# Performance work log

Hardware: AMD Instinct MI355X
Metric: run time of the kernel (lower is better)

Reference implementation:

```python
import jax, jax.numpy as jnp
import numpy as np
from jax import lax

SZ, SENLEN, V, DWE, DPE, MAXPOS, DEE, DR, DC, KLOC = 2048, 128, 50000, 100, 5, 256, 100, 34, 300, 10
CIN = DWE + 2 * DPE + DEE  # 210


def setup_inputs() -> dict:
    key = jax.random.key(0)
    ks = jax.random.split(key, 16)
    inp = jax.random.randint(ks[0], (SZ, SENLEN), 0, V, dtype=jnp.int32)
    pos1 = jax.random.randint(ks[1], (SZ, SENLEN), 0, MAXPOS, dtype=jnp.int32)
    pos2 = jax.random.randint(ks[2], (SZ, SENLEN), 0, MAXPOS, dtype=jnp.int32)
    loc = jax.random.randint(ks[3], (SZ, KLOC), 0, V, dtype=jnp.int32)
    loc_mark = jax.random.randint(ks[4], (SZ,), 1, 6, dtype=jnp.int32)  # 1..5, keeps 4+mark < KLOC
    subtype = jax.random.randint(ks[5], (SZ,), 0, DR, dtype=jnp.int32)
    # piecewise L/M/R sentence masks around two cut points
    a = jax.random.randint(ks[6], (SZ, 1), 1, SENLEN // 2, dtype=jnp.int32)
    b = jax.random.randint(ks[7], (SZ, 1), SENLEN // 2, SENLEN - 1, dtype=jnp.int32)
    ar = jnp.arange(SENLEN)[None, :]
    maskL = (ar < a).astype(jnp.float32)
    maskM = ((ar >= a) & (ar < b)).astype(jnp.float32)
    maskR = (ar >= b).astype(jnp.float32)
    word_emb = 0.1 * jax.random.normal(ks[8], (V, DWE), dtype=jnp.float32)
    pos_emb = 0.1 * jax.random.normal(ks[9], (MAXPOS, DPE), dtype=jnp.float32)
    event_emb = 0.1 * jax.random.normal(ks[10], (DR, DEE), dtype=jnp.float32)
    conv_w = (1.0 / np.sqrt(CIN * 3)) * jax.random.normal(ks[11], (DC, CIN, 3), dtype=jnp.float32)
    conv_b = 0.01 * jax.random.normal(ks[12], (DC,), dtype=jnp.float32)
    return dict(inp=inp, pos1=pos1, pos2=pos2, loc=loc, loc_mark=loc_mark, subtype=subtype,
                maskL=maskL, maskM=maskM, maskR=maskR, word_emb=word_emb, pos_emb=pos_emb,
                event_emb=event_emb, conv_w=conv_w, conv_b=conv_b)


def reference(inp, pos1, pos2, loc, loc_mark, subtype, maskL, maskM, maskR,
              word_emb, pos_emb, event_emb, conv_w, conv_b):
    # padding_idx=0 semantics
    W = word_emb.at[0].set(0.0)
    E = event_emb.at[0].set(0.0)

    embeds = W[inp]                       # (SZ, L, DWE)
    p1 = pos_emb[pos1]                    # (SZ, L, DPE)
    p2 = pos_emb[pos2]                    # (SZ, L, DPE)

    # ragged loc feature: l[4] <- mean(l[4:4+mark]); l[5] <- l[4+mark]; keep l[0:6]
    loc_e = W[loc]                        # (SZ, K, DWE)
    j = jnp.arange(KLOC)[None, :]
    sel = ((j >= 4) & (j < 4 + loc_mark[:, None])).astype(loc_e.dtype)  # (SZ, K)
    mean4 = jnp.einsum('skd,sk->sd', loc_e, sel) / loc_mark[:, None].astype(loc_e.dtype)
    new5 = jnp.take_along_axis(loc_e, (4 + loc_mark)[:, None, None], axis=1)[:, 0, :]
    loc_embeds = jnp.concatenate([loc_e[:, :4].reshape(loc_e.shape[0], -1), mean4, new5], axis=1)  # (SZ, 6*DWE)

    ev = jnp.broadcast_to(E[subtype][:, None, :], (subtype.shape[0], SENLEN, DEE))
    x = jnp.concatenate([embeds, p1, p2, ev], axis=2).transpose(0, 2, 1)  # (SZ, CIN, L)

    conved = lax.conv_general_dilated(x, conv_w, window_strides=(1,), padding=((1, 1),),
                                      dimension_numbers=('NCH', 'OIH', 'NCH'))
    conved = conved + conv_b[None, :, None]  # (SZ, DC, L)

    # (mask*x + 1) -> maxpool over L -> -1  ==  max over L of mask*x (the +/-1 cancels exactly)
    pooledL = jnp.max(conved * maskL[:, None, :], axis=2)
    pooledM = jnp.max(conved * maskM[:, None, :], axis=2)
    pooledR = jnp.max(conved * maskR[:, None, :], axis=2)
    pooled = jnp.concatenate([pooledL, pooledM, pooledR], axis=1)  # (SZ, 3*DC)

    rep = jnp.tanh(jnp.concatenate([pooled, loc_embeds], axis=1))  # dropout in eval = identity
    return rep
```

## Files before the change

### kernel.cpp

```cpp
#include <hip/hip_runtime.h>
#include <hip/hip_bf16.h>

#define SZ    2048
#define SLEN  128
#define DWE   100
#define DPE   5
#define DEE   100
#define DC    300
#define CIN   210
#define KLOC  10
#define OUTW  1500
#define DR    34

#define KP    128
#define LCOLS 136
#define LROWS 130
#define CPAD  320

typedef short short8 __attribute__((ext_vector_type(8)));
typedef float f32x4 __attribute__((ext_vector_type(4)));

static __device__ __forceinline__ unsigned short f2b(float f) {
  return __builtin_bit_cast(unsigned short, __float2bfloat16(f));
}

static __device__ __forceinline__ unsigned cvt_pk_bf16(float lo, float hi) {
  unsigned r;
  asm volatile("v_cvt_pk_bf16_f32 %0, %1, %2" : "=v"(r) : "v"(lo), "v"(hi));
  return r;
}

static __device__ __forceinline__ float ftanh(float x) {
  x = fminf(fmaxf(x, -15.f), 15.f);
  float e = __expf(2.0f * x);
  return (e - 1.0f) * __builtin_amdgcn_rcpf(e + 1.0f);
}

__global__ void prep_wk(const float* __restrict__ conv_w, unsigned short* __restrict__ wk) {
  int idx = blockIdx.x * 256 + threadIdx.x;
  if (idx >= 3 * CPAD * KP) return;
  int i  = idx & (KP - 1);
  int c  = (idx / KP) % CPAD;
  int kk = idx / (KP * CPAD);
  float v = 0.f;
  if (c < DC && i < 110) v = conv_w[(c * CIN + i) * 3 + kk];
  wk[idx] = f2b(v);
}

__global__ void prep_ev(const float* __restrict__ conv_w, const float* __restrict__ event_emb,
                        const float* __restrict__ conv_b, float* __restrict__ evconv) {
  int gid = blockIdx.x * 256 + threadIdx.x;
  int o = gid >> 2, sub = gid & 3;
  if (o >= DR * 3 * DC) return;
  int c  = o % DC;
  int kk = (o / DC) % 3;
  int st = o / (3 * DC);
  float v = 0.f;
  if (st != 0) {
    const float* wrow = conv_w + (c * CIN + 110) * 3 + kk;
    const float* e = event_emb + st * DEE;
    #pragma unroll
    for (int i = 0; i < 25; ++i) v += wrow[3 * (sub * 25 + i)] * e[sub * 25 + i];
  }
  v += __shfl_xor(v, 1);
  v += __shfl_xor(v, 2);
  if (sub == 0) evconv[o] = v + (kk == 1 ? conv_b[c] : 0.f);
}

__global__ __launch_bounds__(512, 4) void dmcnn_main(
    const int* __restrict__ inp, const int* __restrict__ pos1, const int* __restrict__ pos2,
    const int* __restrict__ loc, const int* __restrict__ loc_mark, const int* __restrict__ subtype,
    const float* __restrict__ maskL, const float* __restrict__ maskM, const float* __restrict__ maskR,
    const float* __restrict__ word_emb, const float* __restrict__ pos_emb,
    const unsigned short* __restrict__ wk, const float* __restrict__ evconv,
    float* __restrict__ out)
{
  __shared__ unsigned short XT[LROWS * LCOLS];
  __shared__ float pool[2 * CPAD * 4];
  __shared__ int cw[4];

  const int s   = blockIdx.x;
  const int tid = threadIdx.x;

  if (tid < 64)        ((unsigned*)XT)[tid] = 0u;
  else if (tid < 128)  ((unsigned*)(XT + 129 * LCOLS))[tid - 64] = 0u;

  if (tid < 128) {
    const int inL = maskL[s * SLEN + tid] > 0.5f;
    const int inM = maskM[s * SLEN + tid] > 0.5f;
    unsigned long long bL = __ballot(inL);
    unsigned long long bM = __ballot(inM);
    if ((tid & 63) == 0) {
      cw[tid >> 6]       = __popcll(bL);
      cw[2 + (tid >> 6)] = __popcll(bM);
    }
  }

  {
    const int t = tid >> 2, q = tid & 3;
    unsigned short* row = &XT[(t + 1) * LCOLS];
    const int w = inp[s * SLEN + t];
    const float4* wp = (const float4*)(word_emb + (size_t)w * DWE);
    for (int j = q; j < 25; j += 4) {
      float4 v = wp[j];
      unsigned lo = cvt_pk_bf16(v.x, v.y);
      unsigned hi = cvt_pk_bf16(v.z, v.w);
      if (w == 0) { lo = 0u; hi = 0u; }
      *(uint2*)&row[4 * j] = make_uint2(lo, hi);
    }
    if (q == 1 || q == 2) {
      const int p = (q == 1 ? pos1 : pos2)[s * SLEN + t];
      const float* pp = pos_emb + p * DPE;
      #pragma unroll
      for (int d = 0; d < DPE; ++d) row[DWE + (q - 1) * DPE + d] = f2b(pp[d]);
    } else if (q == 3) {
      #pragma unroll
      for (int d = 0; d < 9; ++d) *(unsigned*)&row[110 + 2 * d] = 0u;
    }
  }
  __syncthreads();

  const int wv   = tid >> 6;
  const int wc   = wv & 3, wt = wv >> 2;
  const int lane = tid & 63;
  const int r16  = lane & 15, q16 = lane >> 4;

  f32x4 acc[4][5];
  #pragma unroll
  for (int tt = 0; tt < 4; ++tt)
    #pragma unroll
    for (int ci = 0; ci < 5; ++ci) acc[tt][ci] = (f32x4){0.f, 0.f, 0.f, 0.f};

  const unsigned short* wbase = wk + (size_t)(80 * wc + r16) * KP + q16 * 8;
  #pragma unroll 1
  for (int ks = 0; ks < 12; ++ks) {
    const int kk = ks >> 2, kt = ks & 3;
    short8 wf[5];
    #pragma unroll
    for (int ci = 0; ci < 5; ++ci)
      wf[ci] = *(const short8*)(wbase + (size_t)(kk * CPAD + 16 * ci) * KP + kt * 32);
    #pragma unroll
    for (int tt = 0; tt < 4; ++tt) {
      short8 xf = *(const short8*)&XT[(64 * wt + 16 * tt + r16 + kk) * LCOLS + kt * 32 + q16 * 8];
      #pragma unroll
      for (int ci = 0; ci < 5; ++ci)
        acc[tt][ci] = __builtin_amdgcn_mfma_f32_16x16x32_bf16(xf, wf[ci], acc[tt][ci], 0, 0, 0);
    }
  }

  const int acut = cw[0] + cw[1];
  const int bcut = acut + cw[2] + cw[3];
  const int st   = subtype[s];
  const float* evc = evconv + (size_t)st * 3 * DC;
  float* orow = out + (size_t)s * OUTW;

  #pragma unroll
  for (int ci = 0; ci < 5; ++ci) {
    const int c = 80 * wc + 16 * ci + r16;
    const int cc = c < DC ? c : 0;
    const float s0 = evc[cc], s1 = evc[cc + DC], s2 = evc[cc + 2 * DC];
    const float base = s0 + s1 + s2;
    float rL = 0.f, rM = 0.f, rR = 0.f;
    #pragma unroll
    for (int tt = 0; tt < 4; ++tt) {
      #pragma unroll
      for (int j = 0; j < 4; ++j) {
        const int t = 64 * wt + 16 * tt + 4 * q16 + j;
        float v = acc[tt][ci][j] + base;
        if (t == 0)   v -= s0;
        if (t == 127) v -= s2;
        if (t < acut)      rL = fmaxf(rL, v);
        else if (t < bcut) rM = fmaxf(rM, v);
        else               rR = fmaxf(rR, v);
      }
    }
    #pragma unroll
    for (int off = 16; off < 64; off <<= 1) {
      rL = fmaxf(rL, __shfl_xor(rL, off));
      rM = fmaxf(rM, __shfl_xor(rM, off));
      rR = fmaxf(rR, __shfl_xor(rR, off));
    }
    if (q16 == 0) {
      float* p = pool + ((size_t)wt * CPAD + c) * 4;
      p[0] = rL; p[1] = rM; p[2] = rR;
    }
  }

  __syncthreads();
  if (tid < DC) {
    const float* p0 = pool + (size_t)tid * 4;
    const float* p1 = pool + (size_t)(CPAD + tid) * 4;
    orow[tid]          = ftanh(fmaxf(p0[0], p1[0]));
    orow[DC + tid]     = ftanh(fmaxf(p0[1], p1[1]));
    orow[2 * DC + tid] = ftanh(fmaxf(p0[2], p1[2]));
  }

  const int mark = loc_mark[s];
  for (int j = tid; j < 600; j += 512) {
    float v;
    if (j < 400) {
      const int k = j / 100, d = j % 100;
      const int idx = loc[s * KLOC + k];
      v = (idx == 0) ? 0.f : word_emb[(size_t)idx * DWE + d];
    } else if (j < 500) {
      const int d = j - 400;
      float sum = 0.f;
      for (int k = 4; k < 4 + mark; ++k) {
        const int idx = loc[s * KLOC + k];
        sum += (idx == 0) ? 0.f : word_emb[(size_t)idx * DWE + d];
      }
      v = sum / (float)mark;
    } else {
      const int d = j - 500;
      const int idx = loc[s * KLOC + 4 + mark];
      v = (idx == 0) ? 0.f : word_emb[(size_t)idx * DWE + d];
    }
    orow[900 + j] = ftanh(v);
  }
}

extern "C" void kernel_launch(void* const* d_in, const int* in_sizes, int n_in,
                              void* d_out, int out_size, void* d_ws, size_t ws_size,
                              hipStream_t stream) {
  const int*   inp       = (const int*)d_in[0];
  const int*   pos1      = (const int*)d_in[1];
  const int*   pos2      = (const int*)d_in[2];
  const int*   loc       = (const int*)d_in[3];
  const int*   loc_mark  = (const int*)d_in[4];
  const int*   subtype   = (const int*)d_in[5];
  const float* maskL     = (const float*)d_in[6];
  const float* maskM     = (const float*)d_in[7];
  const float* maskR     = (const float*)d_in[8];
  const float* word_emb  = (const float*)d_in[9];
  const float* pos_emb   = (const float*)d_in[10];
  const float* event_emb = (const float*)d_in[11];
  const float* conv_w    = (const float*)d_in[12];
  const float* conv_b    = (const float*)d_in[13];

  unsigned short* wk = (unsigned short*)d_ws;
  float* evconv = (float*)((char*)d_ws + 3 * CPAD * KP * 2);
  float* out = (float*)d_out;

  prep_wk<<<(3 * CPAD * KP + 255) / 256, 256, 0, stream>>>(conv_w, wk);
  prep_ev<<<(DR * 3 * DC * 4 + 255) / 256, 256, 0, stream>>>(conv_w, event_emb, conv_b, evconv);
  dmcnn_main<<<SZ, 512, 0, stream>>>(inp, pos1, pos2, loc, loc_mark, subtype,
      maskL, maskM, maskR, word_emb, pos_emb, wk, evconv, out);
}
```

Baseline: 248.2 us.

## Process multiple sentences per block with software-pipelined gathers and separate loc kernel

The main kernel becomes persistent-style: each block handles eight sentences in sequence, prefetching the next sentence's embedding rows, position embeddings, masks and subtype into registers while the MFMA convolution of the current one runs. The loc-feature tanh work moves to its own elementwise kernel, and launch bounds drop to two blocks per CU. This is meant to hide gather latency and amortise block setup, but the grid shrinks to 256 blocks, which may leave CUs underused, and the prefetch registers add pressure.

Result: slower. 273.6 us (+10.2%).

```diff
diff --git a/kernel.cpp b/kernel.cpp
--- a/kernel.cpp
+++ b/kernel.cpp
@@ -16,6 +16,7 @@
 #define LCOLS 136
 #define LROWS 130
 #define CPAD  320
+#define G     8
 
 typedef short short8 __attribute__((ext_vector_type(8)));
 typedef float f32x4 __attribute__((ext_vector_type(4)));
@@ -67,155 +68,226 @@
   if (sub == 0) evconv[o] = v + (kk == 1 ? conv_b[c] : 0.f);
 }
 
-__global__ __launch_bounds__(512, 4) void dmcnn_main(
+__global__ void loc_kernel(const int* __restrict__ loc, const int* __restrict__ loc_mark,
+                           const float* __restrict__ word_emb, float* __restrict__ out) {
+  int gid = blockIdx.x * 256 + threadIdx.x;
+  if (gid >= SZ * 600) return;
+  int s = gid / 600, j = gid % 600;
+  const int mark = loc_mark[s];
+  float v;
+  if (j < 400) {
+    const int k = j / 100, d = j % 100;
+    const int idx = loc[s * KLOC + k];
+    v = (idx == 0) ? 0.f : word_emb[(size_t)idx * DWE + d];
+  } else if (j < 500) {
+    const int d = j - 400;
+    float sum = 0.f;
+    for (int k = 4; k < 4 + mark; ++k) {
+      const int idx = loc[s * KLOC + k];
+      sum += (idx == 0) ? 0.f : word_emb[(size_t)idx * DWE + d];
+    }
+    v = sum / (float)mark;
+  } else {
+    const int d = j - 500;
+    const int idx = loc[s * KLOC + 4 + mark];
+    v = (idx == 0) ? 0.f : word_emb[(size_t)idx * DWE + d];
+  }
+  out[(size_t)s * OUTW + 900 + j] = ftanh(v);
+}
+
+__global__ __launch_bounds__(512, 2) void dmcnn_main(
     const int* __restrict__ inp, const int* __restrict__ pos1, const int* __restrict__ pos2,
-    const int* __restrict__ loc, const int* __restrict__ loc_mark, const int* __restrict__ subtype,
-    const float* __restrict__ maskL, const float* __restrict__ maskM, const float* __restrict__ maskR,
+    const int* __restrict__ subtype,
+    const float* __restrict__ maskL, const float* __restrict__ maskM,
     const float* __restrict__ word_emb, const float* __restrict__ pos_emb,
     const unsigned short* __restrict__ wk, const float* __restrict__ evconv,
     float* __restrict__ out)
 {
   __shared__ unsigned short XT[LROWS * LCOLS];
-  __shared__ float pool[2 * CPAD * 4];
-  __shared__ int cw[4];
-
-  const int s   = blockIdx.x;
+  __shared__ float pool[2 * 304 * 3];
+  __shared__ int cwbuf[2][4];
+
   const int tid = threadIdx.x;
-
-  if (tid < 64)        ((unsigned*)XT)[tid] = 0u;
-  else if (tid < 128)  ((unsigned*)(XT + 129 * LCOLS))[tid - 64] = 0u;
-
-  if (tid < 128) {
-    const int inL = maskL[s * SLEN + tid] > 0.5f;
-    const int inM = maskM[s * SLEN + tid] > 0.5f;
-    unsigned long long bL = __ballot(inL);
-    unsigned long long bM = __ballot(inM);
-    if ((tid & 63) == 0) {
-      cw[tid >> 6]       = __popcll(bL);
-      cw[2 + (tid >> 6)] = __popcll(bM);
-    }
-  }
+  const int t = tid >> 2, q = tid & 3;
+  const int wv = tid >> 6, wc = wv & 3, wt = wv >> 2;
+  const int lane = tid & 63, r16 = lane & 15, q16 = lane >> 4;
+  const int s0 = blockIdx.x * G;
+
+  if (tid < 64)       ((unsigned*)XT)[tid] = 0u;
+  else if (tid < 128) ((unsigned*)(XT + 129 * LCOLS))[tid - 64] = 0u;
+  for (int i = tid; i < 128 * 9; i += 512) {
+    int rr = i / 9, dd = i % 9;
+    *(unsigned*)&XT[(rr + 1) * LCOLS + 110 + 2 * dd] = 0u;
+  }
+
+  int w_stage = inp[s0 * SLEN + t];
+  int p_stage = 0;
+  if (q == 1)      p_stage = pos1[s0 * SLEN + t];
+  else if (q == 2) p_stage = pos2[s0 * SLEN + t];
+  float mLs = 0.f, mMs = 0.f;
+  if (tid < 128) { mLs = maskL[s0 * SLEN + tid]; mMs = maskM[s0 * SLEN + tid]; }
+  int st_cur = subtype[s0];
+  int st_nxt = subtype[s0 + 1];
 
   {
-    const int t = tid >> 2, q = tid & 3;
+    const float4* wp = (const float4*)(word_emb + (size_t)w_stage * DWE);
+    float4 v0[7];
+    #pragma unroll
+    for (int jj = 0; jj < 7; ++jj) { int j = q + 4 * jj; if (j < 25) v0[jj] = wp[j]; }
+    float pv0[5];
+    if (q == 1 || q == 2) {
+      const float* pp = pos_emb + p_stage * DPE;
+      #pragma unroll
+      for (int d = 0; d < 5; ++d) pv0[d] = pp[d];
+    }
     unsigned short* row = &XT[(t + 1) * LCOLS];
-    const int w = inp[s * SLEN + t];
-    const float4* wp = (const float4*)(word_emb + (size_t)w * DWE);
-    for (int j = q; j < 25; j += 4) {
-      float4 v = wp[j];
-      unsigned lo = cvt_pk_bf16(v.x, v.y);
-      unsigned hi = cvt_pk_bf16(v.z, v.w);
-      if (w == 0) { lo = 0u; hi = 0u; }
-      *(uint2*)&row[4 * j] = make_uint2(lo, hi);
+    #pragma unroll
+    for (int jj = 0; jj < 7; ++jj) {
+      int j = q + 4 * jj;
+      if (j < 25) {
+        unsigned lo = cvt_pk_bf16(v0[jj].x, v0[jj].y);
+        unsigned hi = cvt_pk_bf16(v0[jj].z, v0[jj].w);
+        if (w_stage == 0) { lo = 0u; hi = 0u; }
+        *(uint2*)&row[4 * j] = make_uint2(lo, hi);
+      }
     }
     if (q == 1 || q == 2) {
-      const int p = (q == 1 ? pos1 : pos2)[s * SLEN + t];
-      const float* pp = pos_emb + p * DPE;
-      #pragma unroll
-      for (int d = 0; d < DPE; ++d) row[DWE + (q - 1) * DPE + d] = f2b(pp[d]);
-    } else if (q == 3) {
-      #pragma unroll
-      for (int d = 0; d < 9; ++d) *(unsigned*)&row[110 + 2 * d] = 0u;
-    }
+      #pragma unroll
+      for (int d = 0; d < 5; ++d) row[DWE + (q - 1) * DPE + d] = f2b(pv0[d]);
+    }
+    if (tid < 128) {
+      unsigned long long bL = __ballot(mLs > 0.5f);
+      unsigned long long bM = __ballot(mMs > 0.5f);
+      if ((tid & 63) == 0) {
+        cwbuf[0][tid >> 6]       = __popcll(bL);
+        cwbuf[0][2 + (tid >> 6)] = __popcll(bM);
+      }
+    }
+    w_stage = inp[(s0 + 1) * SLEN + t];
+    if (q == 1)      p_stage = pos1[(s0 + 1) * SLEN + t];
+    else if (q == 2) p_stage = pos2[(s0 + 1) * SLEN + t];
+    if (tid < 128) { mLs = maskL[(s0 + 1) * SLEN + tid]; mMs = maskM[(s0 + 1) * SLEN + tid]; }
   }
   __syncthreads();
 
-  const int wv   = tid >> 6;
-  const int wc   = wv & 3, wt = wv >> 2;
-  const int lane = tid & 63;
-  const int r16  = lane & 15, q16 = lane >> 4;
-
-  f32x4 acc[4][5];
-  #pragma unroll
-  for (int tt = 0; tt < 4; ++tt)
-    #pragma unroll
-    for (int ci = 0; ci < 5; ++ci) acc[tt][ci] = (f32x4){0.f, 0.f, 0.f, 0.f};
-
   const unsigned short* wbase = wk + (size_t)(80 * wc + r16) * KP + q16 * 8;
+  float4 v[7];
+  float pv[5];
+
   #pragma unroll 1
-  for (int ks = 0; ks < 12; ++ks) {
-    const int kk = ks >> 2, kt = ks & 3;
-    short8 wf[5];
-    #pragma unroll
-    for (int ci = 0; ci < 5; ++ci)
-      wf[ci] = *(const short8*)(wbase + (size_t)(kk * CPAD + 16 * ci) * KP + kt * 32);
-    #pragma unroll
-    for (int tt = 0; tt < 4; ++tt) {
-      short8 xf = *(const short8*)&XT[(64 * wt + 16 * tt + r16 + kk) * LCOLS + kt * 32 + q16 * 8];
+  for (int g = 0; g < G; ++g) {
+    if (g + 1 < G) {
+      const float4* wp = (const float4*)(word_emb + (size_t)w_stage * DWE);
+      #pragma unroll
+      for (int jj = 0; jj < 7; ++jj) { int j = q + 4 * jj; if (j < 25) v[jj] = wp[j]; }
+      if (q == 1 || q == 2) {
+        const float* pp = pos_emb + p_stage * DPE;
+        #pragma unroll
+        for (int d = 0; d < 5; ++d) pv[d] = pp[d];
+      }
+    }
+
+    f32x4 acc[4][5];
+    #pragma unroll
+    for (int tt = 0; tt < 4; ++tt)
+      #pragma unroll
+      for (int ci = 0; ci < 5; ++ci) acc[tt][ci] = (f32x4){0.f, 0.f, 0.f, 0.f};
+
+    #pragma unroll 1
+    for (int ks = 0; ks < 12; ++ks) {
+      const int kk = ks >> 2, kt = ks & 3;
+      short8 wf[5];
       #pragma unroll
       for (int ci = 0; ci < 5; ++ci)
-        acc[tt][ci] = __builtin_amdgcn_mfma_f32_16x16x32_bf16(xf, wf[ci], acc[tt][ci], 0, 0, 0);
-    }
-  }
-
-  const int acut = cw[0] + cw[1];
-  const int bcut = acut + cw[2] + cw[3];
-  const int st   = subtype[s];
-  const float* evc = evconv + (size_t)st * 3 * DC;
-  float* orow = out + (size_t)s * OUTW;
-
-  #pragma unroll
-  for (int ci = 0; ci < 5; ++ci) {
-    const int c = 80 * wc + 16 * ci + r16;
-    const int cc = c < DC ? c : 0;
-    const float s0 = evc[cc], s1 = evc[cc + DC], s2 = evc[cc + 2 * DC];
-    const float base = s0 + s1 + s2;
-    float rL = 0.f, rM = 0.f, rR = 0.f;
-    #pragma unroll
-    for (int tt = 0; tt < 4; ++tt) {
-      #pragma unroll
-      for (int j = 0; j < 4; ++j) {
-        const int t = 64 * wt + 16 * tt + 4 * q16 + j;
-        float v = acc[tt][ci][j] + base;
-        if (t == 0)   v -= s0;
-        if (t == 127) v -= s2;
-        if (t < acut)      rL = fmaxf(rL, v);
-        else if (t < bcut) rM = fmaxf(rM, v);
-        else               rR = fmaxf(rR, v);
-      }
-    }
-    #pragma unroll
-    for (int off = 16; off < 64; off <<= 1) {
-      rL = fmaxf(rL, __shfl_xor(rL, off));
-      rM = fmaxf(rM, __shfl_xor(rM, off));
-      rR = fmaxf(rR, __shfl_xor(rR, off));
-    }
-    if (q16 == 0) {
-      float* p = pool + ((size_t)wt * CPAD + c) * 4;
-      p[0] = rL; p[1] = rM; p[2] = rR;
-    }
-  }
-
-  __syncthreads();
-  if (tid < DC) {
-    const float* p0 = pool + (size_t)tid * 4;
-    const float* p1 = pool + (size_t)(CPAD + tid) * 4;
-    orow[tid]          = ftanh(fmaxf(p0[0], p1[0]));
-    orow[DC + tid]     = ftanh(fmaxf(p0[1], p1[1]));
-    orow[2 * DC + tid] = ftanh(fmaxf(p0[2], p1[2]));
-  }
-
-  const int mark = loc_mark[s];
-  for (int j = tid; j < 600; j += 512) {
-    float v;
-    if (j < 400) {
-      const int k = j / 100, d = j % 100;
-      const int idx = loc[s * KLOC + k];
-      v = (idx == 0) ? 0.f : word_emb[(size_t)idx * DWE + d];
-    } else if (j < 500) {
-      const int d = j - 400;
-      float sum = 0.f;
-      for (int k = 4; k < 4 + mark; ++k) {
-        const int idx = loc[s * KLOC + k];
-        sum += (idx == 0) ? 0.f : word_emb[(size_t)idx * DWE + d];
-      }
-      v = sum / (float)mark;
-    } else {
-      const int d = j - 500;
-      const int idx = loc[s * KLOC + 4 + mark];
-      v = (idx == 0) ? 0.f : word_emb[(size_t)idx * DWE + d];
-    }
-    orow[900 + j] = ftanh(v);
+        wf[ci] = *(const short8*)(wbase + (size_t)(kk * CPAD + 16 * ci) * KP + kt * 32);
+      #pragma unroll
+      for (int tt = 0; tt < 4; ++tt) {
+        short8 xf = *(const short8*)&XT[(64 * wt + 16 * tt + r16 + kk) * LCOLS + kt * 32 + q16 * 8];
+        #pragma unroll
+        for (int ci = 0; ci < 5; ++ci)
+          acc[tt][ci] = __builtin_amdgcn_mfma_f32_16x16x32_bf16(xf, wf[ci], acc[tt][ci], 0, 0, 0);
+      }
+    }
+
+    const int acut = cwbuf[g & 1][0] + cwbuf[g & 1][1];
+    const int bcut = acut + cwbuf[g & 1][2] + cwbuf[g & 1][3];
+    const float* evc = evconv + (size_t)st_cur * 3 * DC;
+
+    #pragma unroll
+    for (int ci = 0; ci < 5; ++ci) {
+      const int c = 80 * wc + 16 * ci + r16;
+      const int cc = c < DC ? c : 0;
+      const float e0 = evc[cc], e1 = evc[cc + DC], e2 = evc[cc + 2 * DC];
+      const float base = e0 + e1 + e2;
+      float rL = 0.f, rM = 0.f, rR = 0.f;
+      #pragma unroll
+      for (int tt = 0; tt < 4; ++tt) {
+        #pragma unroll
+        for (int j = 0; j < 4; ++j) {
+          const int tt_abs = 64 * wt + 16 * tt + 4 * q16 + j;
+          float x = acc[tt][ci][j] + base;
+          if (tt_abs == 0)   x -= e0;
+          if (tt_abs == 127) x -= e2;
+          if (tt_abs < acut)      rL = fmaxf(rL, x);
+          else if (tt_abs < bcut) rM = fmaxf(rM, x);
+          else                    rR = fmaxf(rR, x);
+        }
+      }
+      #pragma unroll
+      for (int off = 16; off < 64; off <<= 1) {
+        rL = fmaxf(rL, __shfl_xor(rL, off));
+        rM = fmaxf(rM, __shfl_xor(rM, off));
+        rR = fmaxf(rR, __shfl_xor(rR, off));
+      }
+      if (q16 == 0 && c < DC) {
+        float* p = pool + ((size_t)wt * 304 + c) * 3;
+        p[0] = rL; p[1] = rM; p[2] = rR;
+      }
+    }
+    if (g + 1 < G && tid < 128) {
+      unsigned long long bL = __ballot(mLs > 0.5f);
+      unsigned long long bM = __ballot(mMs > 0.5f);
+      if ((tid & 63) == 0) {
+        cwbuf[(g + 1) & 1][tid >> 6]       = __popcll(bL);
+        cwbuf[(g + 1) & 1][2 + (tid >> 6)] = __popcll(bM);
+      }
+    }
+    __syncthreads();
+
+    float* orow = out + (size_t)(s0 + g) * OUTW;
+    if (tid < DC) {
+      const float* p0 = pool + (size_t)tid * 3;
+      const float* p1 = pool + (size_t)(304 + tid) * 3;
+      orow[tid]          = ftanh(fmaxf(p0[0], p1[0]));
+      orow[DC + tid]     = ftanh(fmaxf(p0[1], p1[1]));
+      orow[2 * DC + tid] = ftanh(fmaxf(p0[2], p1[2]));
+    }
+    if (g + 1 < G) {
+      unsigned short* row = &XT[(t + 1) * LCOLS];
+      #pragma unroll
+      for (int jj = 0; jj < 7; ++jj) {
+        int j = q + 4 * jj;
+        if (j < 25) {
+          unsigned lo = cvt_pk_bf16(v[jj].x, v[jj].y);
+          unsigned hi = cvt_pk_bf16(v[jj].z, v[jj].w);
+          if (w_stage == 0) { lo = 0u; hi = 0u; }
+          *(uint2*)&row[4 * j] = make_uint2(lo, hi);
+        }
+      }
+      if (q == 1 || q == 2) {
+        #pragma unroll
+        for (int d = 0; d < 5; ++d) row[DWE + (q - 1) * DPE + d] = f2b(pv[d]);
+      }
+      st_cur = st_nxt;
+      if (g + 2 < G) {
+        w_stage = inp[(s0 + g + 2) * SLEN + t];
+        if (q == 1)      p_stage = pos1[(s0 + g + 2) * SLEN + t];
+        else if (q == 2) p_stage = pos2[(s0 + g + 2) * SLEN + t];
+        if (tid < 128) { mLs = maskL[(s0 + g + 2) * SLEN + tid]; mMs = maskM[(s0 + g + 2) * SLEN + tid]; }
+        st_nxt = subtype[s0 + g + 2];
+      }
+    }
+    __syncthreads();
   }
 }
 
@@ -230,7 +302,6 @@
   const int*   subtype   = (const int*)d_in[5];
   const float* maskL     = (const float*)d_in[6];
   const float* maskM     = (const float*)d_in[7];
-  const float* maskR     = (const float*)d_in[8];
   const float* word_emb  = (const float*)d_in[9];
   const float* pos_emb   = (const float*)d_in[10];
   const float* event_emb = (const float*)d_in[11];
@@ -243,6 +314,7 @@
 
   prep_wk<<<(3 * CPAD * KP + 255) / 256, 256, 0, stream>>>(conv_w, wk);
   prep_ev<<<(DR * 3 * DC * 4 + 255) / 256, 256, 0, stream>>>(conv_w, event_emb, conv_b, evconv);
-  dmcnn_main<<<SZ, 512, 0, stream>>>(inp, pos1, pos2, loc, loc_mark, subtype,
-      maskL, maskM, maskR, word_emb, pos_emb, wk, evconv, out);
-}
+  loc_kernel<<<(SZ * 600 + 255) / 256, 256, 0, stream>>>(loc, loc_mark, word_emb, out);
+  dmcnn_main<<<SZ / G, 512, 0, stream>>>(inp, pos1, pos2, subtype,
+      maskL, maskM, word_emb, pos_emb, wk, evconv, out);
+}
```
